# Kernel tuning notes

Hardware: AMD Instinct MI355X
Metric: run time of the kernel (lower is better)

## Reference

```python
import jax, jax.numpy as jnp
import numpy as np
from jax import lax

B, IMG, PATCH, INNER = 8, 224, 16, 4
EMB, MLP_DEPTH, DEPTH, HEADS = 512, 3, 24, 8
Hp = Wp = IMG // PATCH            # 14
N = Hp * Wp                       # 196
D4, D8 = EMB // 4, EMB // 2       # 128, 256
RPE_L = (2 * Hp - 1) * (2 * Wp - 1)  # 729
EPS = 1e-5


def _ln(x, g, b):
    m = jnp.mean(x, -1, keepdims=True)
    v = jnp.mean(jnp.square(x - m), -1, keepdims=True)
    return (x - m) * lax.rsqrt(v + EPS) * g + b


def _mlp(x, w1, b1, w2, b2):
    return jax.nn.gelu(x @ w1 + b1, approximate=False) @ w2 + b2


def _merge(x, ng, nb, rw):
    # merge 2x2 inner patches: dim -> 4*dim, then project to 2*dim
    x = jnp.concatenate([x[..., 0::2, 0::2, :], x[..., 1::2, 0::2, :],
                         x[..., 0::2, 1::2, :], x[..., 1::2, 1::2, :]], axis=-1)
    return _ln(x, ng, nb) @ rw


def _rpe_index():
    coords = np.stack(np.meshgrid(np.arange(Hp), np.arange(Wp), indexing='ij')).reshape(2, -1)
    rel = (coords[:, :, None] - coords[:, None, :]).transpose(1, 2, 0).astype(np.int64)
    rel[:, :, 0] += Hp - 1
    rel[:, :, 1] += Wp - 1
    rel[:, :, 0] *= 2 * Wp - 1
    return jnp.asarray(rel.sum(-1), dtype=jnp.int32)  # [N, N]


def setup_inputs():
    key = jax.random.key(0)
    cnt = [0]
    def rnd(shape, s=0.02):
        cnt[0] += 1
        return jax.random.normal(jax.random.fold_in(key, cnt[0]), shape, jnp.float32) * s
    d = {}
    d['image'] = jax.random.normal(jax.random.fold_in(key, 999), (B, 3, IMG, IMG), jnp.float32)
    d['conv_w'] = rnd((D4, 3, 4, 4)); d['conv_b'] = jnp.zeros((D4,), jnp.float32)
    d['pn_g'] = jnp.ones((D4,), jnp.float32); d['pn_b'] = jnp.zeros((D4,), jnp.float32)
    for pre, dim in (('s1', D4), ('s2', D8)):
        h = dim * 3  # bridge_mlp_ratio = 3
        d[pre + '_ng'] = jnp.ones((MLP_DEPTH, dim), jnp.float32)
        d[pre + '_nb'] = jnp.zeros((MLP_DEPTH, dim), jnp.float32)
        d[pre + '_w1'] = rnd((MLP_DEPTH, dim, h)); d[pre + '_b1'] = jnp.zeros((MLP_DEPTH, h), jnp.float32)
        d[pre + '_w2'] = rnd((MLP_DEPTH, h, dim)); d[pre + '_b2'] = jnp.zeros((MLP_DEPTH, dim), jnp.float32)
    d['pm1_ng'] = jnp.ones((4 * D4,), jnp.float32); d['pm1_nb'] = jnp.zeros((4 * D4,), jnp.float32); d['pm1_rw'] = rnd((4 * D4, 2 * D4))
    d['pm2_ng'] = jnp.ones((4 * D8,), jnp.float32); d['pm2_nb'] = jnp.zeros((4 * D8,), jnp.float32); d['pm2_rw'] = rnd((4 * D8, 2 * D8))
    d['ape'] = rnd((1, N, EMB))
    d['mb_n1g'] = jnp.ones((DEPTH, EMB), jnp.float32); d['mb_n1b'] = jnp.zeros((DEPTH, EMB), jnp.float32)
    d['mb_qkvw'] = rnd((DEPTH, EMB, 3 * EMB)); d['mb_qkvb'] = jnp.zeros((DEPTH, 3 * EMB), jnp.float32)
    d['mb_tab'] = rnd((DEPTH, RPE_L, HEADS))
    d['mb_projw'] = rnd((DEPTH, EMB, EMB)); d['mb_projb'] = jnp.zeros((DEPTH, EMB), jnp.float32)
    d['mb_n2g'] = jnp.ones((DEPTH, EMB), jnp.float32); d['mb_n2b'] = jnp.zeros((DEPTH, EMB), jnp.float32)
    d['mb_w1'] = rnd((DEPTH, EMB, 4 * EMB)); d['mb_b1'] = jnp.zeros((DEPTH, 4 * EMB), jnp.float32)
    d['mb_w2'] = rnd((DEPTH, 4 * EMB, EMB)); d['mb_b2'] = jnp.zeros((DEPTH, EMB), jnp.float32)
    d['rpe_index'] = _rpe_index()
    return d


def _forward(image, conv_w, conv_b, pn_g, pn_b,
             s1_ng, s1_nb, s1_w1, s1_b1, s1_w2, s1_b2,
             pm1_ng, pm1_nb, pm1_rw,
             s2_ng, s2_nb, s2_w1, s2_b1, s2_w2, s2_b2,
             pm2_ng, pm2_nb, pm2_rw, ape,
             mb_n1g, mb_n1b, mb_qkvw, mb_qkvb, mb_tab, mb_projw, mb_projb,
             mb_n2g, mb_n2b, mb_w1, mb_b1, mb_w2, mb_b2, rpe_index):
    # PatchEmbed: 4x4/4 conv then split into 16x16 patches of 4x4 inner patches
    x = lax.conv_general_dilated(image, conv_w, (4, 4), 'VALID',
                                 dimension_numbers=('NCHW', 'OIHW', 'NCHW'))
    x = x + conv_b[None, :, None, None]                       # [B, D4, 56, 56]
    b = x.shape[0]
    x = x.reshape(b, D4, Hp, INNER, Wp, INNER).transpose(0, 2, 4, 3, 5, 1)
    x = x.reshape(b, N, INNER, INNER, D4)
    x = _ln(x, pn_g, pn_b)

    def mlp_step(h, p):
        ng, nb, w1, b1, w2, b2 = p
        return h + _mlp(_ln(h, ng, nb), w1, b1, w2, b2), None

    x, _ = lax.scan(mlp_step, x, (s1_ng, s1_nb, s1_w1, s1_b1, s1_w2, s1_b2))
    x = _merge(x, pm1_ng, pm1_nb, pm1_rw)                     # inner 2x2, dim 256
    x, _ = lax.scan(mlp_step, x, (s2_ng, s2_nb, s2_w1, s2_b1, s2_w2, s2_b2))
    x = _merge(x, pm2_ng, pm2_nb, pm2_rw)                     # inner 1x1, dim 512
    x = x.reshape(b, N, EMB) + ape                            # absolute pos embed

    hd = EMB // HEADS
    scale = hd ** -0.5
    f32 = jnp.finfo(jnp.float32)

    def attn_step(h, p):
        n1g, n1b, qw, qb, tab, pw, pb, n2g, n2b, w1, b1, w2, b2 = p
        y = _ln(h, n1g, n1b)
        qkv = (y @ qw + qb).reshape(b, N, 3, HEADS, hd).transpose(2, 0, 3, 1, 4)
        q, k, v = qkv[0] * scale, qkv[1], qkv[2]
        bias = tab[rpe_index].transpose(2, 0, 1)              # [H, N, N] rpe gather
        a = jnp.einsum('bhqd,bhkd->bhqk', q, k) + bias[None]
        a = jnp.clip(a.astype(jnp.float32), f32.min, f32.max)
        a = jax.nn.softmax(a, axis=-1).astype(h.dtype)
        y = jnp.einsum('bhqk,bhkd->bhqd', a, v).transpose(0, 2, 1, 3).reshape(b, N, EMB)
        h = h + (y @ pw + pb)
        h = h + _mlp(_ln(h, n2g, n2b), w1, b1, w2, b2)
        return h, None

    x, _ = lax.scan(attn_step, x, (mb_n1g, mb_n1b, mb_qkvw, mb_qkvb, mb_tab,
                                   mb_projw, mb_projb, mb_n2g, mb_n2b,
                                   mb_w1, mb_b1, mb_w2, mb_b2))
    return x


def reference(image, conv_w, conv_b, pn_g, pn_b,
              s1_ng, s1_nb, s1_w1, s1_b1, s1_w2, s1_b2,
              pm1_ng, pm1_nb, pm1_rw,
              s2_ng, s2_nb, s2_w1, s2_b1, s2_w2, s2_b2,
              pm2_ng, pm2_nb, pm2_rw, ape,
              mb_n1g, mb_n1b, mb_qkvw, mb_qkvb, mb_tab, mb_projw, mb_projb,
              mb_n2g, mb_n2b, mb_w1, mb_b1, mb_w2, mb_b2, rpe_index):
    return _forward(image, conv_w, conv_b, pn_g, pn_b,
                    s1_ng, s1_nb, s1_w1, s1_b1, s1_w2, s1_b2,
                    pm1_ng, pm1_nb, pm1_rw,
                    s2_ng, s2_nb, s2_w1, s2_b1, s2_w2, s2_b2,
                    pm2_ng, pm2_nb, pm2_rw, ape,
                    mb_n1g, mb_n1b, mb_qkvw, mb_qkvb, mb_tab, mb_projw, mb_projb,
                    mb_n2g, mb_n2b, mb_w1, mb_b1, mb_w2, mb_b2, rpe_index)
```

## Files before the change

kernel.cpp:

```cpp
#include <hip/hip_runtime.h>
#include <hip/hip_bf16.h>

#define Bb    8
#define IMG   224
#define Hp    14
#define Np    196
#define D4    128
#define D8    256
#define EMB   512
#define HEADS 8
#define RPEL  729
#define DEPTH 24
#define EPS   1e-5f

constexpr int EPI_NONE = 0, EPI_BIAS = 1, EPI_BIAS_GELU = 2, EPI_BIAS_RES = 3, EPI_ATOMIC = 4;

typedef __bf16 bf16x8 __attribute__((ext_vector_type(8)));
typedef float  f32x4  __attribute__((ext_vector_type(4)));

static __device__ __forceinline__ void gload16(const void* g, void* l) {
    __builtin_amdgcn_global_load_lds(
        (const __attribute__((address_space(1))) void*)g,
        (__attribute__((address_space(3))) void*)l, 16, 0, 0);
}

__global__ __launch_bounds__(128) void conv_ln_kernel(
    const float* __restrict__ img, const float* __restrict__ cw,
    const float* __restrict__ cb,  const float* __restrict__ png,
    const float* __restrict__ pnb, float* __restrict__ xout)
{
    int p = blockIdx.x;
    int b = p / 3136, rem = p % 3136;
    int hh = rem / 56, ww = rem % 56;
    __shared__ float win[48];
    __shared__ float red[4];
    int t = threadIdx.x;
    if (t < 48) {
        int ic = t >> 4, kh = (t >> 2) & 3, kw = t & 3;
        win[t] = img[(((size_t)b*3 + ic)*224 + hh*4 + kh)*224 + ww*4 + kw];
    }
    __syncthreads();
    float acc = cb[t];
    const float* wrow = cw + (size_t)t * 48;
    #pragma unroll
    for (int r = 0; r < 48; ++r) acc += win[r] * wrow[r];
    float s = acc, ss = acc * acc;
    #pragma unroll
    for (int o = 32; o > 0; o >>= 1) { s += __shfl_xor(s, o, 64); ss += __shfl_xor(ss, o, 64); }
    int wv = t >> 6;
    if ((t & 63) == 0) { red[wv*2] = s; red[wv*2+1] = ss; }
    __syncthreads();
    s = red[0] + red[2]; ss = red[1] + red[3];
    float mean = s * (1.f/128.f);
    float rstd = rsqrtf(ss * (1.f/128.f) - mean*mean + EPS);
    float v = (acc - mean) * rstd * png[t] + pnb[t];
    int hp = hh >> 2, ih = hh & 3, wp = ww >> 2, iw = ww & 3;
    int bn = b * Np + hp * Hp + wp;
    xout[((size_t)bn*16 + ih*4 + iw)*128 + t] = v;
}

__global__ __launch_bounds__(256) void ln_kernel(
    const float* __restrict__ x, const float* __restrict__ g,
    const float* __restrict__ b, __bf16* __restrict__ y, int M, int D)
{
    int wave = threadIdx.x >> 6, lane = threadIdx.x & 63;
    int row = blockIdx.x * 4 + wave;
    if (row >= M) return;
    const float* xr = x + (size_t)row * D;
    float s = 0.f, ss = 0.f;
    for (int i = lane; i < D; i += 64) { float v = xr[i]; s += v; ss += v*v; }
    #pragma unroll
    for (int o = 32; o > 0; o >>= 1) { s += __shfl_xor(s, o, 64); ss += __shfl_xor(ss, o, 64); }
    float inv = 1.f / (float)D;
    float mean = s * inv;
    float rstd = rsqrtf(ss * inv - mean*mean + EPS);
    __bf16* yr = y + (size_t)row * D;
    for (int i = lane; i < D; i += 64)
        yr[i] = (__bf16)((xr[i] - mean) * rstd * g[i] + b[i]);
}

__global__ __launch_bounds__(256) void merge1_ln_kernel(
    const float* __restrict__ x, const float* __restrict__ g,
    const float* __restrict__ b, __bf16* __restrict__ y)
{
    int wave = threadIdx.x >> 6, lane = threadIdx.x & 63;
    int row = blockIdx.x * 4 + wave;
    if (row >= 6272) return;
    int j2 = row & 1, i2 = (row >> 1) & 1, bn = row >> 2;
    float vals[8]; float s = 0.f, ss = 0.f;
    #pragma unroll
    for (int t = 0; t < 8; ++t) {
        int e = lane + t*64;
        int k = e >> 7, c = e & 127;
        int ih = 2*i2 + (k & 1), iw = 2*j2 + (k >> 1);
        float v = x[((size_t)bn*16 + ih*4 + iw)*128 + c];
        vals[t] = v; s += v; ss += v*v;
    }
    #pragma unroll
    for (int o = 32; o > 0; o >>= 1) { s += __shfl_xor(s, o, 64); ss += __shfl_xor(ss, o, 64); }
    float mean = s * (1.f/512.f);
    float rstd = rsqrtf(ss * (1.f/512.f) - mean*mean + EPS);
    __bf16* yr = y + (size_t)row * 512;
    #pragma unroll
    for (int t = 0; t < 8; ++t) {
        int e = lane + t*64;
        yr[e] = (__bf16)((vals[t] - mean) * rstd * g[e] + b[e]);
    }
}

__global__ __launch_bounds__(256) void merge2_ln_kernel(
    const float* __restrict__ x, const float* __restrict__ g,
    const float* __restrict__ b, __bf16* __restrict__ y)
{
    int wave = threadIdx.x >> 6, lane = threadIdx.x & 63;
    int row = blockIdx.x * 4 + wave;
    if (row >= 1568) return;
    float vals[16]; float s = 0.f, ss = 0.f;
    #pragma unroll
    for (int t = 0; t < 16; ++t) {
        int e = lane + t*64;
        int k = e >> 8, c = e & 255;
        float v = x[((size_t)row*4 + (k & 1)*2 + (k >> 1))*256 + c];
        vals[t] = v; s += v; ss += v*v;
    }
    #pragma unroll
    for (int o = 32; o > 0; o >>= 1) { s += __shfl_xor(s, o, 64); ss += __shfl_xor(ss, o, 64); }
    float mean = s * (1.f/1024.f);
    float rstd = rsqrtf(ss * (1.f/1024.f) - mean*mean + EPS);
    __bf16* yr = y + (size_t)row * 1024;
    #pragma unroll
    for (int t = 0; t < 16; ++t) {
        int e = lane + t*64;
        yr[e] = (__bf16)((vals[t] - mean) * rstd * g[e] + b[e]);
    }
}

static __device__ __forceinline__ void tconv_tile(
    const float* __restrict__ in, __bf16* __restrict__ out,
    int R, int C, int tile, float (*t)[33])
{
    int tiles_c = C >> 5;
    int tr = tile / tiles_c, tc = tile - tr * tiles_c;
    int ty = threadIdx.x >> 3, tx = threadIdx.x & 7;
    const float4 v = *(const float4*)&in[(size_t)(tr*32 + ty) * C + (tc*32 + tx*4)];
    t[ty][tx*4+0] = v.x; t[ty][tx*4+1] = v.y; t[ty][tx*4+2] = v.z; t[ty][tx*4+3] = v.w;
    __syncthreads();
    __bf16 o[4];
    #pragma unroll
    for (int j = 0; j < 4; ++j) o[j] = (__bf16)t[tx*4+j][ty];
    *(uint2*)&out[(size_t)(tc*32 + ty) * R + (tr*32 + tx*4)] = *(const uint2*)o;
}

__global__ __launch_bounds__(256) void tconv_kernel(
    const float* __restrict__ in, __bf16* __restrict__ out, int R, int C)
{
    __shared__ float t[32][33];
    size_t off = (size_t)blockIdx.y * R * C;
    tconv_tile(in + off, out + off, R, C, blockIdx.x, t);
}

__global__ __launch_bounds__(256) void layer_tconv_kernel(
    const float* __restrict__ qkvw, const float* __restrict__ projw,
    const float* __restrict__ w1, const float* __restrict__ w2,
    __bf16* __restrict__ LW)
{
    __shared__ float t[32][33];
    int b = blockIdx.x;
    if (b < 768)        tconv_tile(qkvw,  LW,           512, 1536, b,        t);
    else if (b < 1024)  tconv_tile(projw, LW +  786432, 512,  512, b -  768, t);
    else if (b < 2048)  tconv_tile(w1,    LW + 1048576, 512, 2048, b - 1024, t);
    else                tconv_tile(w2,    LW + 2097152, 2048, 512, b - 2048, t);
}

template<int BM, int EPI>
__global__ __launch_bounds__(256) void gemm_kernel(
    const __bf16* __restrict__ A, const __bf16* __restrict__ Bt,
    const float* __restrict__ bias, const float* __restrict__ Rres,
    void* __restrict__ Cv, int M, int N, int K, int kChunk)
{
    constexpr int BF = (BM == 128) ? 4 : 2;
    __shared__ __bf16 As[BM][32];
    __shared__ __bf16 Bs[128][32];
    const int tid = threadIdx.x, lane = tid & 63, wave = tid >> 6;
    const int m0 = blockIdx.y * BM, n0 = blockIdx.x << 7;
    int wm, wn;
    if constexpr (BM == 128) { wm = (wave >> 1) << 6; wn = (wave & 1) << 6; }
    else                     { wm = 0;                wn = wave << 5;       }
    const int q = lane >> 4, mr = lane & 15;
    const int kstart = blockIdx.z * kChunk;
    const int kend   = min(kstart + kChunk, K);

    f32x4 acc[4][BF];
    #pragma unroll
    for (int i = 0; i < 4; ++i)
        #pragma unroll
        for (int j = 0; j < BF; ++j)
            acc[i][j] = (f32x4){0.f, 0.f, 0.f, 0.f};

    const int crow = tid >> 2, ccol = (tid & 3) << 3;
    const __bf16* ag0 = A + (size_t)min(m0 + crow, M - 1) * K + ccol;
    const __bf16* ag1 = ag0;
    if constexpr (BM == 128)
        ag1 = A + (size_t)min(m0 + 64 + crow, M - 1) * K + ccol;
    const __bf16* bg0 = Bt + (size_t)(n0 + crow) * K + ccol;
    const __bf16* bg1 = Bt + (size_t)(n0 + 64 + crow) * K + ccol;
    char* lA = (char*)&As[0][0] + wave * 1024;
    char* lB = (char*)&Bs[0][0] + wave * 1024;

    for (int k0 = kstart; k0 < kend; k0 += 32) {
        gload16(ag0 + k0, lA);
        if constexpr (BM == 128) gload16(ag1 + k0, lA + 4096);
        gload16(bg0 + k0, lB);
        gload16(bg1 + k0, lB + 4096);
        __syncthreads();
        bf16x8 af[4], bfr[BF];
        #pragma unroll
        for (int i = 0; i < 4; ++i)
            af[i] = *(const bf16x8*)&As[wm + i*16 + mr][q*8];
        #pragma unroll
        for (int j = 0; j < BF; ++j)
            bfr[j] = *(const bf16x8*)&Bs[wn + j*16 + mr][q*8];
        #pragma unroll
        for (int i = 0; i < 4; ++i)
            #pragma unroll
            for (int j = 0; j < BF; ++j)
                acc[i][j] = __builtin_amdgcn_mfma_f32_16x16x32_bf16(af[i], bfr[j], acc[i][j], 0, 0, 0);
        __syncthreads();
    }

    const bool addb = (blockIdx.z == 0);
    #pragma unroll
    for (int i = 0; i < 4; ++i) {
        #pragma unroll
        for (int j = 0; j < BF; ++j) {
            const int n = n0 + wn + j*16 + mr;
            float bv = 0.f;
            if constexpr (EPI != EPI_NONE) bv = bias[n];
            #pragma unroll
            for (int r = 0; r < 4; ++r) {
                const int m = m0 + wm + i*16 + q*4 + r;
                if (m < M) {
                    if constexpr (EPI == EPI_ATOMIC) {
                        atomicAdd(&((float*)Cv)[(size_t)m * N + n], acc[i][j][r] + (addb ? bv : 0.f));
                    } else {
                        float v = acc[i][j][r] + bv;
                        if constexpr (EPI == EPI_BIAS_GELU)
                            v = 0.5f * v * (1.f + erff(v * 0.70710678118654752f));
                        if constexpr (EPI == EPI_BIAS_RES)
                            v += Rres[(size_t)m * N + n];
                        if constexpr (EPI == EPI_BIAS || EPI == EPI_BIAS_GELU)
                            ((__bf16*)Cv)[(size_t)m * N + n] = (__bf16)v;
                        else
                            ((float*)Cv)[(size_t)m * N + n] = v;
                    }
                }
            }
        }
    }
}

__global__ __launch_bounds__(256) void attn_kernel(
    const __bf16* __restrict__ qkv, const float* __restrict__ tab,
    const int* __restrict__ rpe, __bf16* __restrict__ y2)
{
    __shared__ __bf16 Vt[64][232];
    __shared__ __bf16 Pl[4][16][232];
    int blk = blockIdx.x;
    int qg = blk & 3, h = (blk >> 2) & 7, b = blk >> 5;
    int tid = threadIdx.x;

    for (int i = tid; i < 196*8; i += 256) {
        int key = i >> 3, seg = i & 7;
        bf16x8 v = *(const bf16x8*)(qkv + ((size_t)(b*Np + key))*1536 + 1024 + h*64 + seg*8);
        #pragma unroll
        for (int j = 0; j < 8; ++j) Vt[seg*8 + j][key] = v[j];
    }
    {
        int d0 = tid >> 2, cs = tid & 3;
        #pragma unroll
        for (int j = 0; j < 9; ++j) Vt[d0][196 + cs*9 + j] = (__bf16)0.f;
    }
    __syncthreads();

    int lane = tid & 63, wave = tid >> 6;
    int T = qg + 4*wave;
    if (T > 12) return;
    int q = lane >> 4, mr = lane & 15;

    if (lane < 36) {
        #pragma unroll
        for (int r = 0; r < 16; ++r) Pl[wave][r][196 + lane] = (__bf16)0.f;
    }

    int qtok = b*Np + min(T*16 + mr, 195);
    const __bf16* qp = qkv + (size_t)qtok*1536 + h*64 + q*8;
    bf16x8 aq0 = *(const bf16x8*)qp;
    bf16x8 aq1 = *(const bf16x8*)(qp + 32);

    f32x4 sacc[13];
    #pragma unroll
    for (int nt = 0; nt < 13; ++nt) {
        int ktok = b*Np + min(nt*16 + mr, 195);
        const __bf16* kp = qkv + (size_t)ktok*1536 + 512 + h*64 + q*8;
        bf16x8 bk0 = *(const bf16x8*)kp;
        bf16x8 bk1 = *(const bf16x8*)(kp + 32);
        f32x4 z = (f32x4){0.f, 0.f, 0.f, 0.f};
        z = __builtin_amdgcn_mfma_f32_16x16x32_bf16(aq0, bk0, z, 0, 0, 0);
        sacc[nt] = __builtin_amdgcn_mfma_f32_16x16x32_bf16(aq1, bk1, z, 0, 0, 0);
    }

    #pragma unroll
    for (int r = 0; r < 4; ++r) {
        int qi = T*16 + q*4 + r;
        const int* rrow = rpe + (size_t)min(qi, 195) * 196;
        float vals[13];
        #pragma unroll
        for (int nt = 0; nt < 13; ++nt) {
            int col = nt*16 + mr;
            float bv = tab[rrow[min(col, 195)]*8 + h];
            float v = sacc[nt][r] * 0.125f + bv;
            vals[nt] = (col < 196) ? v : -3.0e38f;
        }
        float m = vals[0];
        #pragma unroll
        for (int nt = 1; nt < 13; ++nt) m = fmaxf(m, vals[nt]);
        #pragma unroll
        for (int o = 8; o > 0; o >>= 1) m = fmaxf(m, __shfl_xor(m, o, 64));
        float s = 0.f, p[13];
        #pragma unroll
        for (int nt = 0; nt < 13; ++nt) { p[nt] = __expf(vals[nt] - m); s += p[nt]; }
        #pragma unroll
        for (int o = 8; o > 0; o >>= 1) s += __shfl_xor(s, o, 64);
        float inv = 1.f / s;
        #pragma unroll
        for (int nt = 0; nt < 13; ++nt)
            Pl[wave][q*4 + r][nt*16 + mr] = (__bf16)(p[nt] * inv);
    }

    f32x4 oacc[4];
    #pragma unroll
    for (int nt = 0; nt < 4; ++nt) oacc[nt] = (f32x4){0.f, 0.f, 0.f, 0.f};
    #pragma unroll
    for (int ks = 0; ks < 7; ++ks) {
        bf16x8 ap = *(const bf16x8*)&Pl[wave][mr][ks*32 + q*8];
        #pragma unroll
        for (int nt = 0; nt < 4; ++nt) {
            bf16x8 bv = *(const bf16x8*)&Vt[nt*16 + mr][ks*32 + q*8];
            oacc[nt] = __builtin_amdgcn_mfma_f32_16x16x32_bf16(ap, bv, oacc[nt], 0, 0, 0);
        }
    }

    #pragma unroll
    for (int nt = 0; nt < 4; ++nt) {
        #pragma unroll
        for (int r = 0; r < 4; ++r) {
            int qi = T*16 + q*4 + r;
            if (qi < 196)
                y2[((size_t)(b*Np + qi))*512 + h*64 + nt*16 + mr] = (__bf16)oacc[nt][r];
        }
    }
}

__global__ __launch_bounds__(256) void add_ape_kernel(float* __restrict__ x,
                                                      const float* __restrict__ ape)
{
    int i = blockIdx.x * 256 + threadIdx.x;
    if (i < 1568*512) x[i] += ape[i % (Np*512)];
}

extern "C" void kernel_launch(void* const* d_in, const int* in_sizes, int n_in,
                              void* d_out, int out_size, void* d_ws, size_t ws_size,
                              hipStream_t stream)
{
    typedef const float* fp;
    fp image  = (fp)d_in[0];
    fp conv_w = (fp)d_in[1];  fp conv_b = (fp)d_in[2];
    fp pn_g   = (fp)d_in[3];  fp pn_b   = (fp)d_in[4];
    fp s1_ng  = (fp)d_in[5];  fp s1_nb  = (fp)d_in[6];
    fp s1_w1  = (fp)d_in[7];  fp s1_b1  = (fp)d_in[8];
    fp s1_w2  = (fp)d_in[9];  fp s1_b2  = (fp)d_in[10];
    fp s2_ng  = (fp)d_in[11]; fp s2_nb  = (fp)d_in[12];
    fp s2_w1  = (fp)d_in[13]; fp s2_b1  = (fp)d_in[14];
    fp s2_w2  = (fp)d_in[15]; fp s2_b2  = (fp)d_in[16];
    fp pm1_ng = (fp)d_in[17]; fp pm1_nb = (fp)d_in[18]; fp pm1_rw = (fp)d_in[19];
    fp pm2_ng = (fp)d_in[20]; fp pm2_nb = (fp)d_in[21]; fp pm2_rw = (fp)d_in[22];
    fp ape    = (fp)d_in[23];
    fp n1g    = (fp)d_in[24]; fp n1b    = (fp)d_in[25];
    fp qkvw   = (fp)d_in[26]; fp qkvb   = (fp)d_in[27];
    fp tab    = (fp)d_in[28];
    fp projw  = (fp)d_in[29]; fp projb  = (fp)d_in[30];
    fp n2g    = (fp)d_in[31]; fp n2b    = (fp)d_in[32];
    fp w1     = (fp)d_in[33]; fp b1     = (fp)d_in[34];
    fp w2     = (fp)d_in[35]; fp b2     = (fp)d_in[36];
    const int* rpe = (const int*)d_in[37];

    float*  X  = (float*)d_ws;
    __bf16* H  = (__bf16*)(X + 3211264);
    __bf16* Y  = H + 9633792;
    __bf16* SW = Y + 3211264;
    __bf16* LW = SW + 2129920;

    tconv_kernel<<<dim3(48, 3),  256, 0, stream>>>(s1_w1,  SW + 0,       128, 384);
    tconv_kernel<<<dim3(48, 3),  256, 0, stream>>>(s1_w2,  SW + 147456,  384, 128);
    tconv_kernel<<<dim3(192, 3), 256, 0, stream>>>(s2_w1,  SW + 294912,  256, 768);
    tconv_kernel<<<dim3(192, 3), 256, 0, stream>>>(s2_w2,  SW + 884736,  768, 256);
    tconv_kernel<<<dim3(128, 1), 256, 0, stream>>>(pm1_rw, SW + 1474560, 512, 256);
    tconv_kernel<<<dim3(512, 1), 256, 0, stream>>>(pm2_rw, SW + 1605632, 1024, 512);

    conv_ln_kernel<<<Bb*56*56, 128, 0, stream>>>(image, conv_w, conv_b, pn_g, pn_b, X);

    for (int t = 0; t < 3; ++t) {
        ln_kernel<<<25088/4, 256, 0, stream>>>(X, s1_ng + t*128, s1_nb + t*128, Y, 25088, 128);
        gemm_kernel<128, EPI_BIAS_GELU><<<dim3(3, 196), 256, 0, stream>>>(
            Y, SW + t*49152, s1_b1 + t*384, nullptr, H, 25088, 384, 128, 128);
        gemm_kernel<64, EPI_BIAS_RES><<<dim3(1, 392), 256, 0, stream>>>(
            H, SW + 147456 + t*49152, s1_b2 + t*128, X, X, 25088, 128, 384, 384);
    }
    merge1_ln_kernel<<<6272/4, 256, 0, stream>>>(X, pm1_ng, pm1_nb, Y);
    gemm_kernel<64, EPI_NONE><<<dim3(2, 98), 256, 0, stream>>>(
        Y, SW + 1474560, nullptr, nullptr, X, 6272, 256, 512, 512);
    for (int t = 0; t < 3; ++t) {
        ln_kernel<<<6272/4, 256, 0, stream>>>(X, s2_ng + t*256, s2_nb + t*256, Y, 6272, 256);
        gemm_kernel<128, EPI_BIAS_GELU><<<dim3(6, 49), 256, 0, stream>>>(
            Y, SW + 294912 + t*196608, s2_b1 + t*768, nullptr, H, 6272, 768, 256, 256);
        gemm_kernel<64, EPI_BIAS_RES><<<dim3(2, 98), 256, 0, stream>>>(
            H, SW + 884736 + t*196608, s2_b2 + t*256, X, X, 6272, 256, 768, 768);
    }
    merge2_ln_kernel<<<1568/4, 256, 0, stream>>>(X, pm2_ng, pm2_nb, Y);
    gemm_kernel<64, EPI_NONE><<<dim3(4, 25), 256, 0, stream>>>(
        Y, SW + 1605632, nullptr, nullptr, X, 1568, 512, 1024, 1024);
    add_ape_kernel<<<(1568*512+255)/256, 256, 0, stream>>>(X, ape);

    for (int l = 0; l < DEPTH; ++l) {
        layer_tconv_kernel<<<3072, 256, 0, stream>>>(
            qkvw + (size_t)l*512*1536, projw + (size_t)l*512*512,
            w1 + (size_t)l*512*2048, w2 + (size_t)l*2048*512, LW);
        ln_kernel<<<392, 256, 0, stream>>>(X, n1g + l*EMB, n1b + l*EMB, Y, 1568, EMB);
        gemm_kernel<64, EPI_BIAS><<<dim3(12, 25), 256, 0, stream>>>(
            Y, LW, qkvb + (size_t)l*1536, nullptr, H, 1568, 1536, EMB, EMB);
        attn_kernel<<<256, 256, 0, stream>>>(H, tab + (size_t)l*RPEL*HEADS, rpe, Y);
        gemm_kernel<64, EPI_ATOMIC><<<dim3(4, 25, 4), 256, 0, stream>>>(
            Y, LW + 786432, projb + (size_t)l*EMB, nullptr, X, 1568, EMB, EMB, 128);
        ln_kernel<<<392, 256, 0, stream>>>(X, n2g + l*EMB, n2b + l*EMB, Y, 1568, EMB);
        gemm_kernel<64, EPI_BIAS_GELU><<<dim3(16, 25), 256, 0, stream>>>(
            Y, LW + 1048576, b1 + (size_t)l*2048, nullptr, H, 1568, 2048, EMB, EMB);
        gemm_kernel<64, EPI_ATOMIC><<<dim3(4, 25, 4), 256, 0, stream>>>(
            H, LW + 2097152, b2 + (size_t)l*EMB, nullptr, X, 1568, EMB, 2048, 512);
    }
    hipMemcpyAsync(d_out, X, (size_t)1568*512*sizeof(float), hipMemcpyDeviceToDevice, stream);
}
```

Before: 2.994 ms.

## Add 64x64 GEMM kernel, batch all-layer weight conversion, fuse APE add

Adds a gemm64 kernel that uses 64x64 output tiles, a K-step of 64 and an XOR-swizzled LDS layout. It replaces the older GEMM in the merge and transformer-layer matmuls, which roughly doubles the block count for these small-M GEMMs. When the workspace is large enough, all 24 layers' weights are transposed to bf16 in one upfront launch using 64x64 tiles, removing the per-layer conversion launches. The positional-embedding add is folded into the merge2 GEMM epilogue, dropping a separate elementwise kernel. The trade-offs are a larger workspace and more redundant A-tile loads from the smaller N tiles.

```diff
diff --git a/kernel.cpp b/kernel.cpp
--- a/kernel.cpp
+++ b/kernel.cpp
@@ -13,7 +13,7 @@
 #define DEPTH 24
 #define EPS   1e-5f
 
-constexpr int EPI_NONE = 0, EPI_BIAS = 1, EPI_BIAS_GELU = 2, EPI_BIAS_RES = 3, EPI_ATOMIC = 4;
+constexpr int EPI_NONE = 0, EPI_BIAS = 1, EPI_BIAS_GELU = 2, EPI_BIAS_RES = 3, EPI_ATOMIC = 4, EPI_APE = 5;
 
 typedef __bf16 bf16x8 __attribute__((ext_vector_type(8)));
 typedef float  f32x4  __attribute__((ext_vector_type(4)));
@@ -159,17 +159,49 @@
     tconv_tile(in + off, out + off, R, C, blockIdx.x, t);
 }
 
+static __device__ __forceinline__ void tconv64_tile(
+    const float* __restrict__ in, __bf16* __restrict__ out,
+    int R, int C, int tile, float (*t)[65])
+{
+    int tiles_c = C >> 6;
+    int tr = tile / tiles_c, tc = tile - tr * tiles_c;
+    int tid = threadIdx.x;
+    int lrow = tid >> 4, lcol = (tid & 15) << 2;
+    #pragma unroll
+    for (int i = 0; i < 4; ++i) {
+        int row = lrow + i*16;
+        const float4 v = *(const float4*)&in[(size_t)(tr*64 + row) * C + (tc*64 + lcol)];
+        t[row][lcol+0] = v.x; t[row][lcol+1] = v.y; t[row][lcol+2] = v.z; t[row][lcol+3] = v.w;
+    }
+    __syncthreads();
+    int orow = tid >> 3, och = tid & 7;
+    #pragma unroll
+    for (int i = 0; i < 2; ++i) {
+        int r = orow + i*32;
+        __bf16 o[8];
+        #pragma unroll
+        for (int j = 0; j < 8; ++j) o[j] = (__bf16)t[och*8 + j][r];
+        *(uint4*)&out[(size_t)(tc*64 + r) * R + (tr*64 + och*8)] = *(const uint4*)o;
+    }
+}
+
 __global__ __launch_bounds__(256) void layer_tconv_kernel(
     const float* __restrict__ qkvw, const float* __restrict__ projw,
     const float* __restrict__ w1, const float* __restrict__ w2,
-    __bf16* __restrict__ LW)
-{
-    __shared__ float t[32][33];
+    __bf16* __restrict__ LW, size_t lw_stride)
+{
+    __shared__ float t[64][65];
+    int l = blockIdx.y;
     int b = blockIdx.x;
-    if (b < 768)        tconv_tile(qkvw,  LW,           512, 1536, b,        t);
-    else if (b < 1024)  tconv_tile(projw, LW +  786432, 512,  512, b -  768, t);
-    else if (b < 2048)  tconv_tile(w1,    LW + 1048576, 512, 2048, b - 1024, t);
-    else                tconv_tile(w2,    LW + 2097152, 2048, 512, b - 2048, t);
+    const float* q_ = qkvw  + (size_t)l * 786432;
+    const float* p_ = projw + (size_t)l * 262144;
+    const float* a_ = w1    + (size_t)l * 1048576;
+    const float* c_ = w2    + (size_t)l * 1048576;
+    __bf16* o = LW + (size_t)l * lw_stride;
+    if (b < 192)       tconv64_tile(q_, o,           512, 1536, b,       t);
+    else if (b < 256)  tconv64_tile(p_, o +  786432, 512,  512, b - 192, t);
+    else if (b < 512)  tconv64_tile(a_, o + 1048576, 512, 2048, b - 256, t);
+    else               tconv64_tile(c_, o + 2097152, 2048, 512, b - 512, t);
 }
 
 template<int BM, int EPI>
@@ -259,6 +291,103 @@
     }
 }
 
+template<int EPI>
+__global__ __launch_bounds__(256) void gemm64_kernel(
+    const __bf16* __restrict__ A, const __bf16* __restrict__ Bt,
+    const float* __restrict__ bias, const float* __restrict__ Rres,
+    void* __restrict__ Cv, int M, int N, int K, int kChunk)
+{
+    __shared__ __bf16 As[64][64];
+    __shared__ __bf16 Bs[64][64];
+    const int tid = threadIdx.x, lane = tid & 63, wave = tid >> 6;
+    const int m0 = blockIdx.y << 6, n0 = blockIdx.x << 6;
+    const int wm = (wave >> 1) << 5, wn = (wave & 1) << 5;
+    const int q = lane >> 4, mr = lane & 15;
+    const int kstart = blockIdx.z * kChunk;
+    const int kend   = min(kstart + kChunk, K);
+
+    f32x4 acc[2][2];
+    #pragma unroll
+    for (int i = 0; i < 2; ++i)
+        #pragma unroll
+        for (int j = 0; j < 2; ++j)
+            acc[i][j] = (f32x4){0.f, 0.f, 0.f, 0.f};
+
+    const int srow = tid >> 3;
+    const int scol = ((tid & 7) << 3) ^ ((srow & 7) << 3);
+    const __bf16* agA = A  + (size_t)min(m0 + srow,      M - 1) * K + scol;
+    const __bf16* agB = A  + (size_t)min(m0 + 32 + srow, M - 1) * K + scol;
+    const __bf16* bgA = Bt + (size_t)(n0 + srow)      * K + scol;
+    const __bf16* bgB = Bt + (size_t)(n0 + 32 + srow) * K + scol;
+    char* lA = (char*)&As[0][0] + wave * 1024;
+    char* lB = (char*)&Bs[0][0] + wave * 1024;
+
+    const int pg0 = ((q)     ^ (mr & 7)) << 4;
+    const int pg1 = ((q + 4) ^ (mr & 7)) << 4;
+
+    for (int k0 = kstart; k0 < kend; k0 += 64) {
+        gload16(agA + k0, lA);
+        gload16(agB + k0, lA + 4096);
+        gload16(bgA + k0, lB);
+        gload16(bgB + k0, lB + 4096);
+        __syncthreads();
+        bf16x8 af[2][2], bfr[2][2];
+        #pragma unroll
+        for (int i = 0; i < 2; ++i) {
+            const char* ar = (const char*)&As[wm + i*16 + mr][0];
+            af[i][0] = *(const bf16x8*)(ar + pg0);
+            af[i][1] = *(const bf16x8*)(ar + pg1);
+        }
+        #pragma unroll
+        for (int j = 0; j < 2; ++j) {
+            const char* br = (const char*)&Bs[wn + j*16 + mr][0];
+            bfr[j][0] = *(const bf16x8*)(br + pg0);
+            bfr[j][1] = *(const bf16x8*)(br + pg1);
+        }
+        #pragma unroll
+        for (int i = 0; i < 2; ++i)
+            #pragma unroll
+            for (int j = 0; j < 2; ++j) {
+                acc[i][j] = __builtin_amdgcn_mfma_f32_16x16x32_bf16(af[i][0], bfr[j][0], acc[i][j], 0, 0, 0);
+                acc[i][j] = __builtin_amdgcn_mfma_f32_16x16x32_bf16(af[i][1], bfr[j][1], acc[i][j], 0, 0, 0);
+            }
+        __syncthreads();
+    }
+
+    const bool addb = (blockIdx.z == 0);
+    #pragma unroll
+    for (int i = 0; i < 2; ++i) {
+        #pragma unroll
+        for (int j = 0; j < 2; ++j) {
+            const int n = n0 + wn + j*16 + mr;
+            float bv = 0.f;
+            if constexpr (EPI == EPI_BIAS || EPI == EPI_BIAS_GELU || EPI == EPI_BIAS_RES || EPI == EPI_ATOMIC)
+                bv = bias[n];
+            #pragma unroll
+            for (int r = 0; r < 4; ++r) {
+                const int m = m0 + wm + i*16 + q*4 + r;
+                if (m < M) {
+                    if constexpr (EPI == EPI_ATOMIC) {
+                        atomicAdd(&((float*)Cv)[(size_t)m * N + n], acc[i][j][r] + (addb ? bv : 0.f));
+                    } else {
+                        float v = acc[i][j][r] + bv;
+                        if constexpr (EPI == EPI_BIAS_GELU)
+                            v = 0.5f * v * (1.f + erff(v * 0.70710678118654752f));
+                        if constexpr (EPI == EPI_BIAS_RES)
+                            v += Rres[(size_t)m * N + n];
+                        if constexpr (EPI == EPI_APE)
+                            v += Rres[(size_t)(m % Np) * N + n];
+                        if constexpr (EPI == EPI_BIAS || EPI == EPI_BIAS_GELU)
+                            ((__bf16*)Cv)[(size_t)m * N + n] = (__bf16)v;
+                        else
+                            ((float*)Cv)[(size_t)m * N + n] = v;
+                    }
+                }
+            }
+        }
+    }
+}
+
 __global__ __launch_bounds__(256) void attn_kernel(
     const __bf16* __restrict__ qkv, const float* __restrict__ tab,
     const int* __restrict__ rpe, __bf16* __restrict__ y2)
@@ -359,13 +488,6 @@
                 y2[((size_t)(b*Np + qi))*512 + h*64 + nt*16 + mr] = (__bf16)oacc[nt][r];
         }
     }
-}
-
-__global__ __launch_bounds__(256) void add_ape_kernel(float* __restrict__ x,
-                                                      const float* __restrict__ ape)
-{
-    int i = blockIdx.x * 256 + threadIdx.x;
-    if (i < 1568*512) x[i] += ape[i % (Np*512)];
 }
 
 extern "C" void kernel_launch(void* const* d_in, const int* in_sizes, int n_in,
@@ -400,12 +522,19 @@
     __bf16* SW = Y + 3211264;
     __bf16* LW = SW + 2129920;
 
+    const size_t LWSTRIDE = 3145728;
+    const size_t need_all = ((size_t)(LW - (__bf16*)d_ws)) * 2 + DEPTH * LWSTRIDE * 2;
+    const bool bigLW = ws_size >= need_all;
+
     tconv_kernel<<<dim3(48, 3),  256, 0, stream>>>(s1_w1,  SW + 0,       128, 384);
     tconv_kernel<<<dim3(48, 3),  256, 0, stream>>>(s1_w2,  SW + 147456,  384, 128);
     tconv_kernel<<<dim3(192, 3), 256, 0, stream>>>(s2_w1,  SW + 294912,  256, 768);
     tconv_kernel<<<dim3(192, 3), 256, 0, stream>>>(s2_w2,  SW + 884736,  768, 256);
     tconv_kernel<<<dim3(128, 1), 256, 0, stream>>>(pm1_rw, SW + 1474560, 512, 256);
     tconv_kernel<<<dim3(512, 1), 256, 0, stream>>>(pm2_rw, SW + 1605632, 1024, 512);
+    if (bigLW)
+        layer_tconv_kernel<<<dim3(768, DEPTH), 256, 0, stream>>>(
+            qkvw, projw, w1, w2, LW, LWSTRIDE);
 
     conv_ln_kernel<<<Bb*56*56, 128, 0, stream>>>(image, conv_w, conv_b, pn_g, pn_b, X);
 
@@ -417,7 +546,7 @@
             H, SW + 147456 + t*49152, s1_b2 + t*128, X, X, 25088, 128, 384, 384);
     }
     merge1_ln_kernel<<<6272/4, 256, 0, stream>>>(X, pm1_ng, pm1_nb, Y);
-    gemm_kernel<64, EPI_NONE><<<dim3(2, 98), 256, 0, stream>>>(
+    gemm64_kernel<EPI_NONE><<<dim3(4, 98), 256, 0, stream>>>(
         Y, SW + 1474560, nullptr, nullptr, X, 6272, 256, 512, 512);
     for (int t = 0; t < 3; ++t) {
         ln_kernel<<<6272/4, 256, 0, stream>>>(X, s2_ng + t*256, s2_nb + t*256, Y, 6272, 256);
@@ -427,25 +556,26 @@
             H, SW + 884736 + t*196608, s2_b2 + t*256, X, X, 6272, 256, 768, 768);
     }
     merge2_ln_kernel<<<1568/4, 256, 0, stream>>>(X, pm2_ng, pm2_nb, Y);
-    gemm_kernel<64, EPI_NONE><<<dim3(4, 25), 256, 0, stream>>>(
-        Y, SW + 1605632, nullptr, nullptr, X, 1568, 512, 1024, 1024);
-    add_ape_kernel<<<(1568*512+255)/256, 256, 0, stream>>>(X, ape);
+    gemm64_kernel<EPI_APE><<<dim3(8, 25), 256, 0, stream>>>(
+        Y, SW + 1605632, nullptr, ape, X, 1568, 512, 1024, 1024);
 
     for (int l = 0; l < DEPTH; ++l) {
-        layer_tconv_kernel<<<3072, 256, 0, stream>>>(
-            qkvw + (size_t)l*512*1536, projw + (size_t)l*512*512,
-            w1 + (size_t)l*512*2048, w2 + (size_t)l*2048*512, LW);
+        const __bf16* LWl = bigLW ? LW + (size_t)l * LWSTRIDE : LW;
+        if (!bigLW)
+            layer_tconv_kernel<<<dim3(768, 1), 256, 0, stream>>>(
+                qkvw + (size_t)l*512*1536, projw + (size_t)l*512*512,
+                w1 + (size_t)l*512*2048, w2 + (size_t)l*2048*512, LW, 0);
         ln_kernel<<<392, 256, 0, stream>>>(X, n1g + l*EMB, n1b + l*EMB, Y, 1568, EMB);
-        gemm_kernel<64, EPI_BIAS><<<dim3(12, 25), 256, 0, stream>>>(
-            Y, LW, qkvb + (size_t)l*1536, nullptr, H, 1568, 1536, EMB, EMB);
+        gemm64_kernel<EPI_BIAS><<<dim3(24, 25), 256, 0, stream>>>(
+            Y, LWl, qkvb + (size_t)l*1536, nullptr, H, 1568, 1536, EMB, EMB);
         attn_kernel<<<256, 256, 0, stream>>>(H, tab + (size_t)l*RPEL*HEADS, rpe, Y);
-        gemm_kernel<64, EPI_ATOMIC><<<dim3(4, 25, 4), 256, 0, stream>>>(
-            Y, LW + 786432, projb + (size_t)l*EMB, nullptr, X, 1568, EMB, EMB, 128);
+        gemm64_kernel<EPI_ATOMIC><<<dim3(8, 25, 4), 256, 0, stream>>>(
+            Y, LWl + 786432, projb + (size_t)l*EMB, nullptr, X, 1568, EMB, EMB, 128);
         ln_kernel<<<392, 256, 0, stream>>>(X, n2g + l*EMB, n2b + l*EMB, Y, 1568, EMB);
-        gemm_kernel<64, EPI_BIAS_GELU><<<dim3(16, 25), 256, 0, stream>>>(
-            Y, LW + 1048576, b1 + (size_t)l*2048, nullptr, H, 1568, 2048, EMB, EMB);
-        gemm_kernel<64, EPI_ATOMIC><<<dim3(4, 25, 4), 256, 0, stream>>>(
-            H, LW + 2097152, b2 + (size_t)l*EMB, nullptr, X, 1568, EMB, 2048, 512);
+        gemm64_kernel<EPI_BIAS_GELU><<<dim3(32, 25), 256, 0, stream>>>(
+            Y, LWl + 1048576, b1 + (size_t)l*2048, nullptr, H, 1568, 2048, EMB, EMB);
+        gemm64_kernel<EPI_ATOMIC><<<dim3(8, 25, 4), 256, 0, stream>>>(
+            H, LWl + 2097152, b2 + (size_t)l*EMB, nullptr, X, 1568, EMB, 2048, 512);
     }
     hipMemcpyAsync(d_out, X, (size_t)1568*512*sizeof(float), hipMemcpyDeviceToDevice, stream);
 }
```

New measurement: 2.808 ms. 1.07x faster.
